# Kernel optimization log

Measured on AMD Instinct MI355X. Metric: run time of the kernel, lower is better.

## Reference

```python
import jax, jax.numpy as jnp
import numpy as np

D = 256

def setup_inputs() -> dict:
    key = jax.random.key(0)
    ks = jax.random.split(key, 7)
    B, L, d = 1024, 200, D
    M = jax.random.normal(ks[0], (B, L, d), dtype=jnp.float32)
    N = jax.random.normal(ks[1], (B, L, d), dtype=jnp.float32)
    act_r = jax.random.normal(ks[2], (B, d), dtype=jnp.float32)
    s = 1.0 / np.sqrt(d)
    Wm = jax.random.uniform(ks[3], (d, d), jnp.float32, -s, s)
    bm = jax.random.uniform(ks[4], (d,), jnp.float32, -s, s)
    Wn = jax.random.uniform(ks[5], (d, d), jnp.float32, -s, s)
    bn = jax.random.uniform(ks[6], (d,), jnp.float32, -s, s)
    return {"M": M, "N": N, "act_r": act_r, "Wm": Wm, "bm": bm, "Wn": Wn, "bn": bn}

def _branch(X, W, b, act_r):
    # X: [B,L,d]; Linear + ReLU
    H = jax.nn.relu(jnp.einsum('bld,ed->ble', X, W) + b)
    # attention score against act_r: [B,L]
    scores = jnp.einsum('bld,bd->bl', H, act_r)
    att = jax.nn.softmax(scores, axis=1)  # softmax over L (torch dim=1)
    # (H * att[...,None]).mean over L
    return jnp.einsum('bld,bl->bd', H, att) / X.shape[1]

def reference(M, N, act_r, Wm, bm, Wn, bn):
    m = _branch(M, Wm, bm, act_r)
    n = _branch(N, Wn, bn, act_r)
    return jnp.concatenate((m, n), axis=1)  # [B, 2d]
```

## Files before the change

kernel.cpp:

```cpp
#include <hip/hip_runtime.h>
#include <hip/hip_fp16.h>

typedef _Float16 f16;
typedef f16 f16x8 __attribute__((ext_vector_type(8)));
typedef f16 f16x4 __attribute__((ext_vector_type(4)));
typedef float f32x4 __attribute__((ext_vector_type(4)));

#define D_DIM 256
#define L_DIM 200
#define LPAD 208
#define HSTR 260

__global__ void prep_w16(const float* __restrict__ Wm, const float* __restrict__ Wn,
                         f16* __restrict__ w16) {
    int i = blockIdx.x * 256 + threadIdx.x;
    w16[i] = (f16)Wm[i];
    w16[D_DIM * D_DIM + i] = (f16)Wn[i];
}

__global__ __launch_bounds__(512, 2)
void fused_cls_attn(const float* __restrict__ M, const float* __restrict__ N,
                    const float* __restrict__ act_r,
                    const float* __restrict__ bm, const float* __restrict__ bn,
                    const f16* __restrict__ w16,
                    float* __restrict__ out) {
    const int b  = blockIdx.x;
    const int br = blockIdx.y;
    const float* __restrict__ X    = (br == 0 ? M : N) + (size_t)b * (L_DIM * D_DIM);
    const f16*   __restrict__ W    = w16 + br * (D_DIM * D_DIM);
    const float* __restrict__ bias = (br == 0) ? bm : bn;

    __shared__ f16   Hs[LPAD * HSTR];
    __shared__ float scores[LPAD];
    __shared__ float att[LPAD];
    __shared__ float part[8][D_DIM];
    __shared__ float red[16];

    const int tid  = threadIdx.x;
    const int lane = tid & 63;
    const int wv   = tid >> 6;
    const int r16  = lane & 15;
    const int g    = lane >> 4;

    if (tid < LPAD) scores[tid] = 0.f;

    f16x8 Bf[2][8];
    float arv[2], bv[2];
    #pragma unroll
    for (int nt = 0; nt < 2; ++nt) {
        const int col = wv * 32 + nt * 16 + r16;
        arv[nt] = act_r[b * D_DIM + col];
        bv[nt]  = bias[col];
        #pragma unroll
        for (int ks = 0; ks < 8; ++ks)
            Bf[nt][ks] = *(const f16x8*)(W + col * D_DIM + ks * 32 + g * 8);
    }
    __syncthreads();

    for (int mt = 0; mt < 13; ++mt) {
        const int arow = mt * 16 + r16;
        const float* __restrict__ xr = X + (size_t)(arow < L_DIM ? arow : L_DIM - 1) * D_DIM;
        f16x8 Af[8];
        #pragma unroll
        for (int ks = 0; ks < 8; ++ks) {
            f32x4 x0 = *(const f32x4*)(xr + ks * 32 + g * 8);
            f32x4 x1 = *(const f32x4*)(xr + ks * 32 + g * 8 + 4);
            f16x8 a;
            a[0] = (f16)x0[0]; a[1] = (f16)x0[1]; a[2] = (f16)x0[2]; a[3] = (f16)x0[3];
            a[4] = (f16)x1[0]; a[5] = (f16)x1[1]; a[6] = (f16)x1[2]; a[7] = (f16)x1[3];
            Af[ks] = a;
        }
        float sc[4] = {0.f, 0.f, 0.f, 0.f};
        #pragma unroll
        for (int nt = 0; nt < 2; ++nt) {
            f32x4 acc = {0.f, 0.f, 0.f, 0.f};
            #pragma unroll
            for (int ks = 0; ks < 8; ++ks)
                acc = __builtin_amdgcn_mfma_f32_16x16x32_f16(Af[ks], Bf[nt][ks], acc, 0, 0, 0);
            const int colc = wv * 32 + nt * 16 + r16;
            #pragma unroll
            for (int r = 0; r < 4; ++r) {
                const int rr = mt * 16 + g * 4 + r;
                float h = acc[r] + bv[nt];
                h = h > 0.f ? h : 0.f;
                Hs[rr * HSTR + colc] = (f16)h;
                if (rr < L_DIM) sc[r] += h * arv[nt];
            }
        }
        #pragma unroll
        for (int r = 0; r < 4; ++r) {
            float v = sc[r];
            v += __shfl_xor(v, 1);
            v += __shfl_xor(v, 2);
            v += __shfl_xor(v, 4);
            v += __shfl_xor(v, 8);
            const int rr = mt * 16 + g * 4 + r;
            if (r16 == 0 && rr < L_DIM) atomicAdd(&scores[rr], v);
        }
    }
    __syncthreads();

    const float s = (tid < L_DIM) ? scores[tid] : -3.0e38f;
    float mx = s;
    #pragma unroll
    for (int sh = 32; sh >= 1; sh >>= 1) mx = fmaxf(mx, __shfl_xor(mx, sh));
    if (lane == 0) red[wv] = mx;
    __syncthreads();
    if (tid == 0) {
        float mm = red[0];
        #pragma unroll
        for (int i = 1; i < 8; ++i) mm = fmaxf(mm, red[i]);
        red[8] = mm;
    }
    __syncthreads();
    const float bmax = red[8];
    const float e = (tid < L_DIM) ? __expf(s - bmax) : 0.f;
    if (tid < LPAD) att[tid] = e;
    float z = e;
    #pragma unroll
    for (int sh = 32; sh >= 1; sh >>= 1) z += __shfl_xor(z, sh);
    __syncthreads();
    if (lane == 0) red[wv] = z;
    __syncthreads();
    if (tid == 0) {
        float zz = 0.f;
        #pragma unroll
        for (int i = 0; i < 8; ++i) zz += red[i];
        red[9] = 1.f / (zz * (float)L_DIM);
    }
    __syncthreads();
    const float scale = red[9];

    {
        const int colq = (tid & 63) * 4;
        const int q    = tid >> 6;
        float a0 = 0.f, a1 = 0.f, a2 = 0.f, a3 = 0.f;
        const int l0 = q * 25;
        #pragma unroll
        for (int l = l0; l < l0 + 25; ++l) {
            const float al = att[l];
            f16x4 hv = *(const f16x4*)(&Hs[l * HSTR + colq]);
            a0 += al * (float)hv[0];
            a1 += al * (float)hv[1];
            a2 += al * (float)hv[2];
            a3 += al * (float)hv[3];
        }
        part[q][colq + 0] = a0;
        part[q][colq + 1] = a1;
        part[q][colq + 2] = a2;
        part[q][colq + 3] = a3;
    }
    __syncthreads();
    if (tid < D_DIM) {
        float sum = 0.f;
        #pragma unroll
        for (int qq = 0; qq < 8; ++qq) sum += part[qq][tid];
        out[(size_t)b * (2 * D_DIM) + br * D_DIM + tid] = sum * scale;
    }
}

extern "C" void kernel_launch(void* const* d_in, const int* in_sizes, int n_in,
                              void* d_out, int out_size, void* d_ws, size_t ws_size,
                              hipStream_t stream) {
    const float* M     = (const float*)d_in[0];
    const float* N     = (const float*)d_in[1];
    const float* act_r = (const float*)d_in[2];
    const float* Wm    = (const float*)d_in[3];
    const float* bm    = (const float*)d_in[4];
    const float* Wn    = (const float*)d_in[5];
    const float* bn    = (const float*)d_in[6];
    float* out = (float*)d_out;
    f16* w16 = (f16*)d_ws;

    const int B = in_sizes[2] / D_DIM;

    prep_w16<<<D_DIM * D_DIM / 256, 256, 0, stream>>>(Wm, Wn, w16);
    dim3 grid(B, 2);
    fused_cls_attn<<<grid, 512, 0, stream>>>(M, N, act_r, bm, bn, w16, out);
}
```

Measured before the change: 702.0 us.

## Split sequence into two halves per block with flash-style softmax combine

Each (batch, branch) is split across two blocks over the L dimension, each computing partial weighted sums plus local max and exp-sum, then a small combine kernel merges them with rescaled softmax statistics. Shared memory per block drops, so occupancy rises to 4 blocks per CU. The next row tile's X loads are software-prefetched during MFMAs, and the weight fp16 conversion is folded into the main kernel. The cost is an extra kernel launch, a workspace round-trip, and each block reloading and converting W from fp32.

```diff
diff --git a/kernel.cpp b/kernel.cpp
--- a/kernel.cpp
+++ b/kernel.cpp
@@ -8,31 +8,37 @@
 
 #define D_DIM 256
 #define L_DIM 200
-#define LPAD 208
+#define LROWS_MAX 112
 #define HSTR 260
 
-__global__ void prep_w16(const float* __restrict__ Wm, const float* __restrict__ Wn,
-                         f16* __restrict__ w16) {
-    int i = blockIdx.x * 256 + threadIdx.x;
-    w16[i] = (f16)Wm[i];
-    w16[D_DIM * D_DIM + i] = (f16)Wn[i];
-}
-
-__global__ __launch_bounds__(512, 2)
-void fused_cls_attn(const float* __restrict__ M, const float* __restrict__ N,
-                    const float* __restrict__ act_r,
-                    const float* __restrict__ bm, const float* __restrict__ bn,
-                    const f16* __restrict__ w16,
-                    float* __restrict__ out) {
-    const int b  = blockIdx.x;
-    const int br = blockIdx.y;
-    const float* __restrict__ X    = (br == 0 ? M : N) + (size_t)b * (L_DIM * D_DIM);
-    const f16*   __restrict__ W    = w16 + br * (D_DIM * D_DIM);
-    const float* __restrict__ bias = (br == 0) ? bm : bn;
-
-    __shared__ f16   Hs[LPAD * HSTR];
-    __shared__ float scores[LPAD];
-    __shared__ float att[LPAD];
+__device__ __forceinline__ f16x8 cvt8(f32x4 x0, f32x4 x1) {
+    f16x8 a;
+    a[0] = (f16)x0[0]; a[1] = (f16)x0[1]; a[2] = (f16)x0[2]; a[3] = (f16)x0[3];
+    a[4] = (f16)x1[0]; a[5] = (f16)x1[1]; a[6] = (f16)x1[2]; a[7] = (f16)x1[3];
+    return a;
+}
+
+__global__ __launch_bounds__(512, 4)
+void fused_half(const float* __restrict__ M, const float* __restrict__ N,
+                const float* __restrict__ act_r,
+                const float* __restrict__ Wm, const float* __restrict__ bm,
+                const float* __restrict__ Wn, const float* __restrict__ bn,
+                float* __restrict__ pws) {
+    const int b    = blockIdx.x;
+    const int br   = blockIdx.y;
+    const int half = blockIdx.z;
+    const int NT    = half ? 6  : 7;
+    const int LROWS = half ? 96 : 112;
+    const int VR    = half ? 88 : 112;
+    const int row0  = half ? 112 : 0;
+
+    const float* __restrict__ X    = (br ? N : M) + (size_t)b * (L_DIM * D_DIM);
+    const float* __restrict__ W    = br ? Wn : Wm;
+    const float* __restrict__ bias = br ? bn : bm;
+
+    __shared__ f16   Hs[LROWS_MAX * HSTR];
+    __shared__ float scores[LROWS_MAX];
+    __shared__ float att[LROWS_MAX];
     __shared__ float part[8][D_DIM];
     __shared__ float red[16];
 
@@ -42,7 +48,7 @@
     const int r16  = lane & 15;
     const int g    = lane >> 4;
 
-    if (tid < LPAD) scores[tid] = 0.f;
+    if (tid < LROWS_MAX) scores[tid] = 0.f;
 
     f16x8 Bf[2][8];
     float arv[2], bv[2];
@@ -52,40 +58,58 @@
         arv[nt] = act_r[b * D_DIM + col];
         bv[nt]  = bias[col];
         #pragma unroll
-        for (int ks = 0; ks < 8; ++ks)
-            Bf[nt][ks] = *(const f16x8*)(W + col * D_DIM + ks * 32 + g * 8);
-    }
-    __syncthreads();
-
-    for (int mt = 0; mt < 13; ++mt) {
-        const int arow = mt * 16 + r16;
-        const float* __restrict__ xr = X + (size_t)(arow < L_DIM ? arow : L_DIM - 1) * D_DIM;
-        f16x8 Af[8];
-        #pragma unroll
         for (int ks = 0; ks < 8; ++ks) {
-            f32x4 x0 = *(const f32x4*)(xr + ks * 32 + g * 8);
-            f32x4 x1 = *(const f32x4*)(xr + ks * 32 + g * 8 + 4);
-            f16x8 a;
-            a[0] = (f16)x0[0]; a[1] = (f16)x0[1]; a[2] = (f16)x0[2]; a[3] = (f16)x0[3];
-            a[4] = (f16)x1[0]; a[5] = (f16)x1[1]; a[6] = (f16)x1[2]; a[7] = (f16)x1[3];
-            Af[ks] = a;
-        }
-        float sc[4] = {0.f, 0.f, 0.f, 0.f};
-        #pragma unroll
-        for (int nt = 0; nt < 2; ++nt) {
-            f32x4 acc = {0.f, 0.f, 0.f, 0.f};
+            f32x4 w0 = *(const f32x4*)(W + col * D_DIM + ks * 32 + g * 8);
+            f32x4 w1 = *(const f32x4*)(W + col * D_DIM + ks * 32 + g * 8 + 4);
+            Bf[nt][ks] = cvt8(w0, w1);
+        }
+    }
+    __syncthreads();
+
+    f32x4 R[8];
+    const float* xr = X + (size_t)min(row0 + r16, L_DIM - 1) * D_DIM;
+    #pragma unroll
+    for (int k = 0; k < 4; ++k) {
+        R[2*k]   = *(const f32x4*)(xr + k * 32 + g * 8);
+        R[2*k+1] = *(const f32x4*)(xr + k * 32 + g * 8 + 4);
+    }
+
+    for (int mt = 0; mt < NT; ++mt) {
+        f32x4 acc0 = {0.f, 0.f, 0.f, 0.f}, acc1 = {0.f, 0.f, 0.f, 0.f};
+        #pragma unroll
+        for (int ks = 0; ks < 4; ++ks) {
+            f16x8 a = cvt8(R[2*ks], R[2*ks+1]);
+            acc0 = __builtin_amdgcn_mfma_f32_16x16x32_f16(a, Bf[0][ks], acc0, 0, 0, 0);
+            acc1 = __builtin_amdgcn_mfma_f32_16x16x32_f16(a, Bf[1][ks], acc1, 0, 0, 0);
+        }
+        const float* xr_cur = xr;
+        if (mt + 1 < NT) {
+            const float* xn = X + (size_t)min(row0 + (mt + 1) * 16 + r16, L_DIM - 1) * D_DIM;
             #pragma unroll
-            for (int ks = 0; ks < 8; ++ks)
-                acc = __builtin_amdgcn_mfma_f32_16x16x32_f16(Af[ks], Bf[nt][ks], acc, 0, 0, 0);
-            const int colc = wv * 32 + nt * 16 + r16;
-            #pragma unroll
-            for (int r = 0; r < 4; ++r) {
-                const int rr = mt * 16 + g * 4 + r;
-                float h = acc[r] + bv[nt];
-                h = h > 0.f ? h : 0.f;
-                Hs[rr * HSTR + colc] = (f16)h;
-                if (rr < L_DIM) sc[r] += h * arv[nt];
+            for (int k = 0; k < 4; ++k) {
+                R[2*k]   = *(const f32x4*)(xn + k * 32 + g * 8);
+                R[2*k+1] = *(const f32x4*)(xn + k * 32 + g * 8 + 4);
             }
+            xr = xn;
+        }
+        #pragma unroll
+        for (int ks = 4; ks < 8; ++ks) {
+            f32x4 q0 = *(const f32x4*)(xr_cur + ks * 32 + g * 8);
+            f32x4 q1 = *(const f32x4*)(xr_cur + ks * 32 + g * 8 + 4);
+            f16x8 a = cvt8(q0, q1);
+            acc0 = __builtin_amdgcn_mfma_f32_16x16x32_f16(a, Bf[0][ks], acc0, 0, 0, 0);
+            acc1 = __builtin_amdgcn_mfma_f32_16x16x32_f16(a, Bf[1][ks], acc1, 0, 0, 0);
+        }
+        float sc[4];
+        const int colc = wv * 32 + r16;
+        #pragma unroll
+        for (int r = 0; r < 4; ++r) {
+            const int rr = mt * 16 + g * 4 + r;
+            float h0 = acc0[r] + bv[0]; h0 = h0 > 0.f ? h0 : 0.f;
+            float h1 = acc1[r] + bv[1]; h1 = h1 > 0.f ? h1 : 0.f;
+            Hs[rr * HSTR + colc]      = (f16)h0;
+            Hs[rr * HSTR + colc + 16] = (f16)h1;
+            sc[r] = (rr < VR) ? (h0 * arv[0] + h1 * arv[1]) : 0.f;
         }
         #pragma unroll
         for (int r = 0; r < 4; ++r) {
@@ -95,12 +119,12 @@
             v += __shfl_xor(v, 4);
             v += __shfl_xor(v, 8);
             const int rr = mt * 16 + g * 4 + r;
-            if (r16 == 0 && rr < L_DIM) atomicAdd(&scores[rr], v);
-        }
-    }
-    __syncthreads();
-
-    const float s = (tid < L_DIM) ? scores[tid] : -3.0e38f;
+            if (r16 == 0 && rr < VR) atomicAdd(&scores[rr], v);
+        }
+    }
+    __syncthreads();
+
+    const float s = (tid < VR) ? scores[tid] : -3.0e38f;
     float mx = s;
     #pragma unroll
     for (int sh = 32; sh >= 1; sh >>= 1) mx = fmaxf(mx, __shfl_xor(mx, sh));
@@ -114,8 +138,8 @@
     }
     __syncthreads();
     const float bmax = red[8];
-    const float e = (tid < L_DIM) ? __expf(s - bmax) : 0.f;
-    if (tid < LPAD) att[tid] = e;
+    const float e = (tid < VR) ? __expf(s - bmax) : 0.f;
+    if (tid < LROWS_MAX) att[tid] = e;
     float z = e;
     #pragma unroll
     for (int sh = 32; sh >= 1; sh >>= 1) z += __shfl_xor(z, sh);
@@ -126,18 +150,17 @@
         float zz = 0.f;
         #pragma unroll
         for (int i = 0; i < 8; ++i) zz += red[i];
-        red[9] = 1.f / (zz * (float)L_DIM);
-    }
-    __syncthreads();
-    const float scale = red[9];
+        red[9] = zz;
+    }
+    __syncthreads();
 
     {
         const int colq = (tid & 63) * 4;
         const int q    = tid >> 6;
+        const int rpq  = LROWS >> 3;
         float a0 = 0.f, a1 = 0.f, a2 = 0.f, a3 = 0.f;
-        const int l0 = q * 25;
-        #pragma unroll
-        for (int l = l0; l < l0 + 25; ++l) {
+        const int l0 = q * rpq;
+        for (int l = l0; l < l0 + rpq; ++l) {
             const float al = att[l];
             f16x4 hv = *(const f16x4*)(&Hs[l * HSTR + colq]);
             a0 += al * (float)hv[0];
@@ -151,12 +174,30 @@
         part[q][colq + 3] = a3;
     }
     __syncthreads();
+    float* __restrict__ pw = pws + (((size_t)b * 2 + br) * 2 + half) * 258;
     if (tid < D_DIM) {
         float sum = 0.f;
         #pragma unroll
         for (int qq = 0; qq < 8; ++qq) sum += part[qq][tid];
-        out[(size_t)b * (2 * D_DIM) + br * D_DIM + tid] = sum * scale;
-    }
+        pw[tid] = sum;
+    }
+    if (tid == 256) pw[256] = red[8];
+    if (tid == 257) pw[257] = red[9];
+}
+
+__global__ void combine_halves(const float* __restrict__ pws, float* __restrict__ out) {
+    const int pair = blockIdx.x;
+    const int col  = threadIdx.x;
+    const float* p0 = pws + (size_t)(pair * 2 + 0) * 258;
+    const float* p1 = pws + (size_t)(pair * 2 + 1) * 258;
+    const float m0 = p0[256], z0 = p0[257];
+    const float m1 = p1[256], z1 = p1[257];
+    const float m  = fmaxf(m0, m1);
+    const float e0 = __expf(m0 - m), e1 = __expf(m1 - m);
+    const float zi = 1.f / ((z0 * e0 + z1 * e1) * (float)L_DIM);
+    const float v  = p0[col] * e0 + p1[col] * e1;
+    const int bb = pair >> 1, rb = pair & 1;
+    out[(size_t)bb * (2 * D_DIM) + rb * D_DIM + col] = v * zi;
 }
 
 extern "C" void kernel_launch(void* const* d_in, const int* in_sizes, int n_in,
@@ -170,11 +211,11 @@
     const float* Wn    = (const float*)d_in[5];
     const float* bn    = (const float*)d_in[6];
     float* out = (float*)d_out;
-    f16* w16 = (f16*)d_ws;
+    float* pws = (float*)d_ws;
 
     const int B = in_sizes[2] / D_DIM;
 
-    prep_w16<<<D_DIM * D_DIM / 256, 256, 0, stream>>>(Wm, Wn, w16);
-    dim3 grid(B, 2);
-    fused_cls_attn<<<grid, 512, 0, stream>>>(M, N, act_r, bm, bn, w16, out);
-}
+    dim3 grid(B, 2, 2);
+    fused_half<<<grid, 512, 0, stream>>>(M, N, act_r, Wm, bm, Wn, bn, pws);
+    combine_halves<<<B * 2, D_DIM, 0, stream>>>(pws, out);
+}
```

Result: slower. 766.9 us (+9.3%).
